# Performance work log

Measured on AMD Instinct MI355X. Metric: run time of the kernel, lower is better.

Reference implementation:

```python
import jax, jax.numpy as jnp
import numpy as np

B, D, T, H, CHUNK, MAX_REL = 4, 512, 8192, 8, 64, 2
HD = D // H


def setup_inputs() -> dict:
    key = jax.random.key(0)
    ks = jax.random.split(key, 16)
    s = 0.02
    inp = {
        "q": jax.random.normal(ks[0], (B, D, T), jnp.float32),
        "k": jax.random.normal(ks[1], (B, D, T), jnp.float32),
        "v": jax.random.normal(ks[2], (B, D, T), jnp.float32),
        "masks": jnp.ones((B, 1, T), jnp.float32),
        "Wq": jax.random.normal(ks[3], (D, D), jnp.float32) * s,
        "bq": jnp.zeros((D,), jnp.float32),
        "Wk": jax.random.normal(ks[4], (D, D), jnp.float32) * s,
        "bk": jnp.zeros((D,), jnp.float32),
        "Wv": jax.random.normal(ks[5], (D, D), jnp.float32) * s,
        "bv": jnp.zeros((D,), jnp.float32),
        "Wo": jax.random.normal(ks[6], (D, D), jnp.float32) * s,
        "bo": jnp.zeros((D,), jnp.float32),
        "rel_k": jax.random.normal(ks[7], (2 * MAX_REL + 1, HD), jnp.float32) * s,
        "rel_v": jax.random.normal(ks[8], (2 * MAX_REL + 1, HD), jnp.float32) * s,
    }
    return inp


def reference(q, k, v, masks, Wq, bq, Wk, bk, Wv, bv, Wo, bo, rel_k, rel_v):
    n = CHUNK
    g = T // n  # T is a multiple of chunck_size -> no padding branch
    bg = B * g

    # (B, D, T) -> (B, T, D) -> (B*g, n, D) chunking
    qt = jnp.swapaxes(q, 1, 2).reshape(bg, n, D)
    kt = jnp.swapaxes(k, 1, 2).reshape(bg, n, D)
    vt = jnp.swapaxes(v, 1, 2).reshape(bg, n, D)
    cm = jnp.swapaxes(masks, 1, 2).reshape(bg, n)  # per-chunk mask values

    # gen_key_padding_mask: chunks that are entirely zero are un-masked (set to 1)
    all_zero = jnp.sum(cm, axis=-1) == 0.0
    cm_fixed = jnp.where(all_zero[:, None], 1.0, cm)
    kpm = cm_fixed == 0.0  # (bg, n) True = masked key

    # projections (torch Linear: x @ W.T + b)
    qp = qt @ Wq.T + bq
    kp = kt @ Wk.T + bk
    vp = vt @ Wv.T + bv

    qh = qp.reshape(bg, n, H, HD).transpose(0, 2, 1, 3)  # (bg, H, n, hd)
    kh = kp.reshape(bg, n, H, HD).transpose(0, 2, 1, 3)
    vh = vp.reshape(bg, n, H, HD).transpose(0, 2, 1, 3)

    # content-content scores
    attn1 = jnp.einsum('bhqd,bhkd->bhqk', qh, kh)

    # relative position indices: clip(k - q, -max, max) + max
    ridx = jnp.clip(jnp.arange(n)[None, :] - jnp.arange(n)[:, None], -MAX_REL, MAX_REL) + MAX_REL
    rk = rel_k[ridx]  # (n, n, hd)
    rv = rel_v[ridx]  # (n, n, hd)

    # content-position scores
    attn2 = jnp.einsum('bhqd,qkd->bhqk', qh, rk)

    scale = jnp.sqrt(jnp.asarray(HD, jnp.float32))
    attn = (attn1 + attn2) / scale
    attn = jnp.where(kpm[:, None, None, :], -jnp.inf, attn)
    p = jax.nn.softmax(attn, axis=-1)  # (bg, H, n, n)

    w1 = jnp.einsum('bhqk,bhkd->bhqd', p, vh)
    w2 = jnp.einsum('bhqk,qkd->bhqd', p, rv)
    xo = (w1 + w2).transpose(0, 2, 1, 3).reshape(bg, n, D)
    xo = xo @ Wo.T + bo

    out = xo.reshape(B, T, D)
    out = jnp.swapaxes(out, 1, 2)  # (B, D, T)
    return out * masks
```

## Files before the change

### kernel.cpp

```cpp
#include <hip/hip_runtime.h>


typedef __attribute__((ext_vector_type(8))) short short8;
typedef __attribute__((ext_vector_type(4))) float f32x4;
typedef __attribute__((ext_vector_type(2))) unsigned int uint2v;
typedef __attribute__((ext_vector_type(4))) unsigned short ushort4v;

#define DEV static __device__ __forceinline__

DEV unsigned short f2bf(float f) {
  union { float f; unsigned int u; } x; x.f = f;
  unsigned int r = x.u + 0x7fffu + ((x.u >> 16) & 1u);
  return (unsigned short)(r >> 16);
}
DEV float bf2f(unsigned short h) {
  union { unsigned int u; float f; } x; x.u = ((unsigned int)h) << 16;
  return x.f;
}

constexpr int Bn = 4, Dm = 512, Tn = 8192, NC = 64;
constexpr int Gn = Tn / NC;
constexpr int BG = Bn * Gn;
constexpr int WSZ = Dm * Dm;
constexpr size_t XTSZ = (size_t)Bn * Tn * Dm;

__global__ __launch_bounds__(256) void wcvt_tiled(
    const float* __restrict__ wq, const float* __restrict__ wk,
    const float* __restrict__ wv, const float* __restrict__ wo,
    unsigned short* __restrict__ dst) {
  int i = blockIdx.x * 256 + threadIdx.x;
  int m = i >> 16, fi = i & 65535;
  int o = fi >> 7, d = (fi & 127) << 2;
  const float* src = (m == 0) ? wq : (m == 1) ? wk : (m == 2) ? wv : wo;
  f32x4 v = *(const f32x4*)(src + o * Dm + d);
  ushort4v u;
  u[0] = f2bf(v[0]); u[1] = f2bf(v[1]); u[2] = f2bf(v[2]); u[3] = f2bf(v[3]);
  int doff = m * WSZ + ((o >> 6) << 15) + ((d >> 5) << 11) + ((o & 63) << 5) + (d & 31);
  *(ushort4v*)(dst + doff) = u;
}

__global__ __launch_bounds__(256) void xpose_kernel(
    const float* __restrict__ q, const float* __restrict__ k,
    const float* __restrict__ v, unsigned short* __restrict__ xt) {
  __shared__ unsigned short tile[64 * 65];
  const int tid = threadIdx.x, bid = blockIdx.x;
  const int tz = bid >> 12, rem = bid & 4095;
  const int cid = rem >> 3, dh = rem & 7;
  const int b = cid >> 7, t0 = (cid & 127) * 64, d0 = dh * 64;
  const float* xin = (tz == 0) ? q : (tz == 1) ? k : v;
  const int lane = tid & 63, drow = tid >> 6;
  const size_t base = (size_t)b * Dm * Tn + t0 + lane;
#pragma unroll
  for (int p = 0; p < 16; ++p) {
    int dr = drow + p * 4;
    float f = xin[base + (size_t)(d0 + dr) * Tn];
    tile[lane * 65 + dr] = f2bf(f);
  }
  __syncthreads();
  unsigned short* xb = xt + (size_t)tz * XTSZ + ((size_t)cid << 15) + (dh << 12);
  const int t = tid >> 2, dlo = (tid & 3) * 8;
#pragma unroll
  for (int h = 0; h < 2; ++h) {
    short8 s;
#pragma unroll
    for (int j = 0; j < 8; ++j) s[j] = (short)tile[t * 65 + h * 32 + dlo + j];
    *(short8*)(xb + h * 2048 + t * 32 + dlo) = s;
  }
}

__global__ __launch_bounds__(512, 2)
void fused2_kernel(const unsigned short* __restrict__ xt,
                   const float* __restrict__ masks,
                   const unsigned short* __restrict__ wbf,
                   const float* __restrict__ bq, const float* __restrict__ bk,
                   const float* __restrict__ bv, const float* __restrict__ bo,
                   const float* __restrict__ relk, const float* __restrict__ relv,
                   float* __restrict__ out)
{
  extern __shared__ char lds[];
  const int tid  = threadIdx.x;
  const int lane = tid & 63;
  const int w    = tid >> 6;
  const int l15  = lane & 15;
  const int lg   = lane >> 4;
  const int c    = blockIdx.x;
  const int b    = c >> 7;
  const int t0   = (c & (Gn - 1)) * NC;

  char* regA = lds + w * 16384;
  char* regB = regA + 8192;

  float cmv = masks[(size_t)b * Tn + t0 + lane];
  unsigned long long nzb = __ballot(cmv != 0.0f);
  unsigned long long kpm = (nzb == 0ull) ? 0ull : __ballot(cmv == 0.0f);

  const f32x4 fzero = {0.f, 0.f, 0.f, 0.f};
  const int aoff = l15 * 32 + lg * 8;
  const unsigned short* xq = xt + ((size_t)c << 15);
  const unsigned short* xk = xq + XTSZ;
  const unsigned short* xv = xq + 2 * XTSZ;

  auto project = [&](const unsigned short* __restrict__ xb,
                     const unsigned short* __restrict__ wb, f32x4 (&acc)[4][4]) {
#pragma unroll
    for (int mi = 0; mi < 4; ++mi)
#pragma unroll
      for (int ni = 0; ni < 4; ++ni) acc[mi][ni] = fzero;
#pragma unroll
    for (int kk = 0; kk < 16; ++kk) {
      short8 af[4], bf_[4];
#pragma unroll
      for (int mi = 0; mi < 4; ++mi)
        af[mi] = *(const short8*)(xb + kk * 2048 + mi * 512 + aoff);
#pragma unroll
      for (int ni = 0; ni < 4; ++ni)
        bf_[ni] = *(const short8*)(wb + kk * 2048 + ni * 512 + aoff);
#pragma unroll
      for (int ni = 0; ni < 4; ++ni)
#pragma unroll
        for (int mi = 0; mi < 4; ++mi)
          acc[mi][ni] = __builtin_amdgcn_mfma_f32_16x16x32_bf16(af[mi], bf_[ni],
                                                                acc[mi][ni], 0, 0, 0);
    }
  };

  f32x4 acc[4][4];

  project(xq, wbf + 0 * WSZ + w * 32768, acc);
#pragma unroll
  for (int ni = 0; ni < 4; ++ni) {
    float bia = bq[64 * w + ni * 16 + l15];
    int hd = ni * 16 + l15;
#pragma unroll
    for (int mi = 0; mi < 4; ++mi)
#pragma unroll
      for (int rr = 0; rr < 4; ++rr) {
        int t = mi * 16 + lg * 4 + rr;
        int off = (t * 128 + hd * 2) ^ ((t & 7) << 4);
        *(unsigned short*)(regA + off) = f2bf(acc[mi][ni][rr] + bia);
      }
  }

  project(xk, wbf + 1 * WSZ + w * 32768, acc);
#pragma unroll
  for (int ni = 0; ni < 4; ++ni) {
    float bia = bk[64 * w + ni * 16 + l15];
    int hd = ni * 16 + l15;
#pragma unroll
    for (int mi = 0; mi < 4; ++mi)
// ... 119 lines not shown
#pragma unroll
    for (int ni = 0; ni < 4; ++ni) oacc[mi][ni] = fzero;
#pragma unroll
  for (int kk = 0; kk < 2; ++kk) {
    short8 av[4], bp[4];
#pragma unroll
    for (int mi = 0; mi < 4; ++mi) {
      int row = mi * 16 + l15;
      int off = (row * 128 + (kk * 32 + lg * 8) * 2) ^ ((row & 7) << 4);
      av[mi] = *(const short8*)(regA + off);
      bp[mi] = *(const short8*)(regB + off);
    }
#pragma unroll
    for (int ni = 0; ni < 4; ++ni)
#pragma unroll
      for (int mi = 0; mi < 4; ++mi)
        oacc[mi][ni] = __builtin_amdgcn_mfma_f32_16x16x32_bf16(av[mi], bp[ni],
                                                               oacc[mi][ni], 0, 0, 0);
  }

  float psh0[4], psh1[4], psh2[4], psh3[4], psh4[4];
#pragma unroll
  for (int ni = 0; ni < 4; ++ni) {
    int qt2 = ni * 16 + l15;
    psh0[ni] = __shfl(ps0, qt2); psh1[ni] = __shfl(ps1, qt2); psh2[ni] = __shfl(ps2, qt2);
    psh3[ni] = __shfl(ps3, qt2); psh4[ni] = __shfl(ps4, qt2);
  }
  uint2v xop[4][4];
#pragma unroll
  for (int mi = 0; mi < 4; ++mi) {
    float rv_[4][5];
#pragma unroll
    for (int rr = 0; rr < 4; ++rr) {
      int hd = mi * 16 + lg * 4 + rr;
#pragma unroll
      for (int r = 0; r < 5; ++r) rv_[rr][r] = relv[r * 64 + hd];
    }
#pragma unroll
    for (int ni = 0; ni < 4; ++ni) {
      unsigned short u[4];
#pragma unroll
      for (int rr = 0; rr < 4; ++rr) {
        float w2 = psh0[ni] * rv_[rr][0] + psh1[ni] * rv_[rr][1] + psh2[ni] * rv_[rr][2]
                 + psh3[ni] * rv_[rr][3] + psh4[ni] * rv_[rr][4];
        u[rr] = f2bf(oacc[mi][ni][rr] + w2);
      }
      uint2v pk; pk[0] = u[0] | ((unsigned int)u[1] << 16);
      pk[1] = u[2] | ((unsigned int)u[3] << 16);
      xop[mi][ni] = pk;
    }
  }

  __syncthreads();
  char* xobuf = lds;
#pragma unroll
  for (int ni = 0; ni < 4; ++ni) {
    int t = ni * 16 + l15;
#pragma unroll
    for (int mi = 0; mi < 4; ++mi) {
      int d = 64 * w + mi * 16 + lg * 4;
      int off = (t * 1024 + d * 2) ^ ((t & 15) << 4);
      *(uint2v*)(xobuf + off) = xop[mi][ni];
    }
  }
  __syncthreads();

  f32x4 cacc[4][4];
#pragma unroll
  for (int mi = 0; mi < 4; ++mi)
#pragma unroll
    for (int ni = 0; ni < 4; ++ni) cacc[mi][ni] = fzero;
  const unsigned short* wob = wbf + 3 * WSZ + w * 32768;
#pragma unroll
  for (int kk = 0; kk < 16; ++kk) {
    short8 ax[4], bw[4];
#pragma unroll
    for (int mi = 0; mi < 4; ++mi) {
      int t = mi * 16 + l15;
      int off = (t * 1024 + (kk * 32 + lg * 8) * 2) ^ ((t & 15) << 4);
      ax[mi] = *(const short8*)(xobuf + off);
    }
#pragma unroll
    for (int ni = 0; ni < 4; ++ni)
      bw[ni] = *(const short8*)(wob + kk * 2048 + ni * 512 + aoff);
#pragma unroll
    for (int ni = 0; ni < 4; ++ni)
#pragma unroll
      for (int mi = 0; mi < 4; ++mi)
        cacc[mi][ni] = __builtin_amdgcn_mfma_f32_16x16x32_bf16(ax[mi], bw[ni],
                                                               cacc[mi][ni], 0, 0, 0);
  }
#pragma unroll
  for (int mi = 0; mi < 4; ++mi) {
    int tl = mi * 16 + lg * 4;
    f32x4 mv = *(const f32x4*)(masks + (size_t)b * Tn + t0 + tl);
#pragma unroll
    for (int ni = 0; ni < 4; ++ni) {
      int o = 64 * w + ni * 16 + l15;
      float bia = bo[o];
      f32x4 r;
#pragma unroll
      for (int rr = 0; rr < 4; ++rr) r[rr] = (cacc[mi][ni][rr] + bia) * mv[rr];
      *(f32x4*)(out + ((size_t)b * Dm + o) * Tn + t0 + tl) = r;
    }
  }
}

__global__ void wcvt_kernel(const float* __restrict__ wq, const float* __restrict__ wk,
                            const float* __restrict__ wv, const float* __restrict__ wo,
                            unsigned short* __restrict__ dst) {
  int i = (blockIdx.x * blockDim.x + threadIdx.x) * 4;
  const float* src = (i < WSZ) ? wq : (i < 2 * WSZ) ? wk : (i < 3 * WSZ) ? wv : wo;
  int off = i & (WSZ - 1);
  f32x4 v = *(const f32x4*)(src + off);
  ushort4v o;
  o[0] = f2bf(v[0]); o[1] = f2bf(v[1]); o[2] = f2bf(v[2]); o[3] = f2bf(v[3]);
  *(ushort4v*)(dst + i) = o;
}

__global__ __launch_bounds__(512, 2)
void fused_kernel(const float* __restrict__ qx, const float* __restrict__ kx,
                  const float* __restrict__ vx, const float* __restrict__ masks,
                  const unsigned short* __restrict__ wbf,
                  const float* __restrict__ bq, const float* __restrict__ bk,
                  const float* __restrict__ bv, const float* __restrict__ bo,
                  const float* __restrict__ relk, const float* __restrict__ relv,
                  float* __restrict__ out)
{
  extern __shared__ char lds[];
  const int tid  = threadIdx.x;
  const int lane = tid & 63;
  const int w    = tid >> 6;
  const int l15  = lane & 15;
  const int lg   = lane >> 4;
  const int c    = blockIdx.x;
  const int b    = c >> 7;
  const int t0   = (c & (Gn - 1)) * NC;

  char* xbuf = lds;
  char* regA = lds + 16 * 1024 + w * 16 * 1024;
  char* regB = regA + 8 * 1024;

  float cmv = masks[(size_t)b * Tn + t0 + lane];
  unsigned long long nzb = __ballot(cmv != 0.0f);
  unsigned long long kpm = (nzb == 0ull) ? 0ull : __ballot(cmv == 0.0f);

  const f32x4 fzero = {0.f, 0.f, 0.f, 0.f};

  auto project = [&](const float* __restrict__ xin, const unsigned short* __restrict__ Wp,
                     f32x4 (&acc)[4][4]) {
#pragma unroll
    for (int mi = 0; mi < 4; ++mi)
#pragma unroll
      for (int ni = 0; ni < 4; ++ni) acc[mi][ni] = fzero;
    const size_t xbase = (size_t)b * Dm * Tn + t0 + lane;
    for (int s = 0; s < 4; ++s) {
      const int d0 = s * 128;
      short8 xs[2];
#pragma unroll
      for (int cc = 0; cc < 2; ++cc)
#pragma unroll
        for (int j = 0; j < 8; ++j) {
          float f = xin[xbase + (size_t)(d0 + 16 * w + 8 * cc + j) * Tn];
          xs[cc][j] = (short)f2bf(f);
        }
      short8 wf[4][4];
#pragma unroll
      for (int ni = 0; ni < 4; ++ni)
#pragma unroll
        for (int kk = 0; kk < 4; ++kk) {
          int o = 64 * w + ni * 16 + l15;
          int d = d0 + kk * 32 + lg * 8;
          wf[ni][kk] = *(const short8*)(Wp + o * Dm + d);
        }
      __syncthreads();
#pragma unroll
      for (int cc = 0; cc < 2; ++cc) {
        int off = (lane * 256 + (16 * w + 8 * cc) * 2) ^ ((lane & 15) << 4);
        *(short8*)(xbuf + off) = xs[cc];
      }
      __syncthreads();
#pragma unroll
      for (int kk = 0; kk < 4; ++kk) {
        short8 af[4];
#pragma unroll
        for (int mi = 0; mi < 4; ++mi) {
          int t = mi * 16 + l15;
          int off = (t * 256 + (kk * 32 + lg * 8) * 2) ^ ((t & 15) << 4);
          af[mi] = *(const short8*)(xbuf + off);
        }
#pragma unroll
        for (int ni = 0; ni < 4; ++ni)
#pragma unroll
          for (int mi = 0; mi < 4; ++mi)
            acc[mi][ni] = __builtin_amdgcn_mfma_f32_16x16x32_bf16(af[mi], wf[ni][kk],
                                                                  acc[mi][ni], 0, 0, 0);
      }
    }
  };

  f32x4 acc[4][4];

  project(qx, wbf + 0 * WSZ, acc);
#pragma unroll
  for (int ni = 0; ni < 4; ++ni) {
    float bia = bq[64 * w + ni * 16 + l15];
    int hd = ni * 16 + l15;
#pragma unroll
    for (int mi = 0; mi < 4; ++mi)
#pragma unroll
      for (int rr = 0; rr < 4; ++rr) {
        int t = mi * 16 + lg * 4 + rr;
        int off = (t * 128 + hd * 2) ^ ((t & 7) << 4);
        *(unsigned short*)(regA + off) = f2bf(acc[mi][ni][rr] + bia);
      }
  }

  project(kx, wbf + 1 * WSZ, acc);
#pragma unroll
  for (int ni = 0; ni < 4; ++ni) {
    float bia = bk[64 * w + ni * 16 + l15];
    int hd = ni * 16 + l15;
#pragma unroll
    for (int mi = 0; mi < 4; ++mi)
#pragma unroll
      for (int rr = 0; rr < 4; ++rr) {
        int t = mi * 16 + lg * 4 + rr;
        int off = (t * 128 + hd * 2) ^ ((t & 7) << 4);
        *(unsigned short*)(regB + off) = f2bf(acc[mi][ni][rr] + bia);
      }
  }

  f32x4 sacc[4][4];
#pragma unroll
  for (int mi = 0; mi < 4; ++mi)
#pragma unroll
    for (int ni = 0; ni < 4; ++ni) sacc[mi][ni] = fzero;
#pragma unroll
  for (int kk = 0; kk < 2; ++kk) {
    short8 aq[4], bkf[4];
#pragma unroll
    for (int mi = 0; mi < 4; ++mi) {
      int t = mi * 16 + l15;
      int off = (t * 128 + (kk * 32 + lg * 8) * 2) ^ ((t & 7) << 4);
      aq[mi]  = *(const short8*)(regA + off);
      bkf[mi] = *(const short8*)(regB + off);
    }
#pragma unroll
    for (int ni = 0; ni < 4; ++ni)
#pragma unroll
      for (int mi = 0; mi < 4; ++mi)
        sacc[mi][ni] = __builtin_amdgcn_mfma_f32_16x16x32_bf16(aq[mi], bkf[ni],
                                                               sacc[mi][ni], 0, 0, 0);
  }

  float qr0 = 0, qr1 = 0, qr2 = 0, qr3 = 0, qr4 = 0;
#pragma unroll
  for (int g = 0; g < 8; ++g) {
    short8 q8 = *(const short8*)(regA + ((lane * 128 + g * 16) ^ ((lane & 7) << 4)));
#pragma unroll
    for (int j = 0; j < 8; ++j) {
      float qf = bf2f((unsigned short)q8[j]);
      qr0 += qf * relk[0 * 64 + g * 8 + j];
      qr1 += qf * relk[1 * 64 + g * 8 + j];
      qr2 += qf * relk[2 * 64 + g * 8 + j];
      qr3 += qf * relk[3 * 64 + g * 8 + j];
      qr4 += qf * relk[4 * 64 + g * 8 + j];
    }
  }

  const float scale = 0.125f;
#pragma unroll
  for (int mi = 0; mi < 4; ++mi)
#pragma unroll
    for (int rr = 0; rr < 4; ++rr) {
      int qt = mi * 16 + lg * 4 + rr;
      float q0 = __shfl(qr0, qt), q1 = __shfl(qr1, qt), q2 = __shfl(qr2, qt),
            q3 = __shfl(qr3, qt), q4 = __shfl(qr4, qt);
      float sv[4];
#pragma unroll
      for (int ni = 0; ni < 4; ++ni) {
        int kt = ni * 16 + l15;
        int dd = kt - qt;
        float a2 = (dd <= -2) ? q0 : (dd == -1) ? q1 : (dd == 0) ? q2 : (dd == 1) ? q3 : q4;
        float s = (sacc[mi][ni][rr] + a2) * scale;
        if ((kpm >> kt) & 1ull) s = -1e30f;
        sv[ni] = s;
      }
      float m = fmaxf(fmaxf(sv[0], sv[1]), fmaxf(sv[2], sv[3]));
#pragma unroll
      for (int xm = 1; xm < 16; xm <<= 1) m = fmaxf(m, __shfl_xor(m, xm));
      float ssum = 0.f;
#pragma unroll
      for (int ni = 0; ni < 4; ++ni) { sv[ni] = __expf(sv[ni] - m); ssum += sv[ni]; }
#pragma unroll
      for (int xm = 1; xm < 16; xm <<= 1) ssum += __shfl_xor(ssum, xm);
      float inv = 1.0f / ssum;
#pragma unroll
      for (int ni = 0; ni < 4; ++ni) {
        int kt = ni * 16 + l15;
        int off = (qt * 128 + kt * 2) ^ ((qt & 7) << 4);
        *(unsigned short*)(regB + off) = f2bf(sv[ni] * inv);
      }
    }

  float ps0 = 0, ps1 = 0, ps2 = 0, ps3 = 0, tot = 0;
#pragma unroll
  for (int g = 0; g < 8; ++g) {
    short8 p8 = *(const short8*)(regB + ((lane * 128 + g * 16) ^ ((lane & 7) << 4)));
#pragma unroll
    for (int j = 0; j < 8; ++j) {
      int kt = g * 8 + j;
      float p = bf2f((unsigned short)p8[j]);
      int dd = kt - lane;
      tot += p;
      ps0 += (dd <= -2) ? p : 0.f;
      ps1  = (dd == -1) ? p : ps1;
      ps2  = (dd ==  0) ? p : ps2;
      ps3  = (dd ==  1) ? p : ps3;
    }
  }
  float ps4 = tot - ps0 - ps1 - ps2 - ps3;

  project(vx, wbf + 2 * WSZ, acc);
#pragma unroll
  for (int ni = 0; ni < 4; ++ni) {
    float bia = bv[64 * w + ni * 16 + l15];
    int hd = ni * 16 + l15;
#pragma unroll
    for (int mi = 0; mi < 4; ++mi) {
      unsigned int lo = (unsigned int)f2bf(acc[mi][ni][0] + bia) |
                        ((unsigned int)f2bf(acc[mi][ni][1] + bia) << 16);
      unsigned int hi = (unsigned int)f2bf(acc[mi][ni][2] + bia) |
                        ((unsigned int)f2bf(acc[mi][ni][3] + bia) << 16);
      uint2v pk; pk[0] = lo; pk[1] = hi;
      int off = (hd * 128 + (mi * 16 + lg * 4) * 2) ^ ((hd & 7) << 4);
      *(uint2v*)(regA + off) = pk;
    }
  }

  f32x4 oacc[4][4];
#pragma unroll
  for (int mi = 0; mi < 4; ++mi)
#pragma unroll
    for (int ni = 0; ni < 4; ++ni) oacc[mi][ni] = fzero;
#pragma unroll
  for (int kk = 0; kk < 2; ++kk) {
    short8 av[4], bp[4];
#pragma unroll
    for (int mi = 0; mi < 4; ++mi) {
      int row = mi * 16 + l15;
      int off = (row * 128 + (kk * 32 + lg * 8) * 2) ^ ((row & 7) << 4);
      av[mi] = *(const short8*)(regA + off);
      bp[mi] = *(const short8*)(regB + off);
    }
#pragma unroll
    for (int ni = 0; ni < 4; ++ni)
#pragma unroll
      for (int mi = 0; mi < 4; ++mi)
        oacc[mi][ni] = __builtin_amdgcn_mfma_f32_16x16x32_bf16(av[mi], bp[ni],
                                                               oacc[mi][ni], 0, 0, 0);
  }

  float psh0[4], psh1[4], psh2[4], psh3[4], psh4[4];
#pragma unroll
  for (int ni = 0; ni < 4; ++ni) {
    int qt2 = ni * 16 + l15;
    psh0[ni] = __shfl(ps0, qt2); psh1[ni] = __shfl(ps1, qt2); psh2[ni] = __shfl(ps2, qt2);
    psh3[ni] = __shfl(ps3, qt2); psh4[ni] = __shfl(ps4, qt2);
  }
  uint2v xop[4][4];
#pragma unroll
  for (int mi = 0; mi < 4; ++mi) {
    float rv_[4][5];
#pragma unroll
    for (int rr = 0; rr < 4; ++rr) {
      int hd = mi * 16 + lg * 4 + rr;
#pragma unroll
      for (int r = 0; r < 5; ++r) rv_[rr][r] = relv[r * 64 + hd];
    }
#pragma unroll
    for (int ni = 0; ni < 4; ++ni) {
      unsigned short u[4];
#pragma unroll
      for (int rr = 0; rr < 4; ++rr) {
        float w2 = psh0[ni] * rv_[rr][0] + psh1[ni] * rv_[rr][1] + psh2[ni] * rv_[rr][2]
                 + psh3[ni] * rv_[rr][3] + psh4[ni] * rv_[rr][4];
        u[rr] = f2bf(oacc[mi][ni][rr] + w2);
      }
      uint2v pk; pk[0] = u[0] | ((unsigned int)u[1] << 16);
      pk[1] = u[2] | ((unsigned int)u[3] << 16);
      xop[mi][ni] = pk;
    }
  }

  __syncthreads();
  char* xobuf = lds + 16 * 1024;
#pragma unroll
  for (int ni = 0; ni < 4; ++ni) {
    int t = ni * 16 + l15;
#pragma unroll
    for (int mi = 0; mi < 4; ++mi) {
      int d = 64 * w + mi * 16 + lg * 4;
      int off = (t * 1024 + d * 2) ^ ((t & 15) << 4);
      *(uint2v*)(xobuf + off) = xop[mi][ni];
    }
  }
  __syncthreads();

  f32x4 cacc[4][4];
#pragma unroll
  for (int mi = 0; mi < 4; ++mi)
#pragma unroll
    for (int ni = 0; ni < 4; ++ni) cacc[mi][ni] = fzero;
  const unsigned short* Wo = wbf + 3 * WSZ;
#pragma unroll
  for (int kk = 0; kk < 16; ++kk) {
    short8 ax[4], bw[4];
#pragma unroll
    for (int mi = 0; mi < 4; ++mi) {
      int t = mi * 16 + l15;
      int off = (t * 1024 + (kk * 32 + lg * 8) * 2) ^ ((t & 15) << 4);
      ax[mi] = *(const short8*)(xobuf + off);
    }
#pragma unroll
    for (int ni = 0; ni < 4; ++ni) {
      int o = 64 * w + ni * 16 + l15;
      bw[ni] = *(const short8*)(Wo + o * Dm + kk * 32 + lg * 8);
    }
#pragma unroll
    for (int ni = 0; ni < 4; ++ni)
#pragma unroll
      for (int mi = 0; mi < 4; ++mi)
        cacc[mi][ni] = __builtin_amdgcn_mfma_f32_16x16x32_bf16(ax[mi], bw[ni],
                                                               cacc[mi][ni], 0, 0, 0);
  }
#pragma unroll
  for (int mi = 0; mi < 4; ++mi) {
    int tl = mi * 16 + lg * 4;
    f32x4 mv = *(const f32x4*)(masks + (size_t)b * Tn + t0 + tl);
#pragma unroll
    for (int ni = 0; ni < 4; ++ni) {
      int o = 64 * w + ni * 16 + l15;
      float bia = bo[o];
      f32x4 r;
#pragma unroll
      for (int rr = 0; rr < 4; ++rr) r[rr] = (cacc[mi][ni][rr] + bia) * mv[rr];
      *(f32x4*)(out + ((size_t)b * Dm + o) * Tn + t0 + tl) = r;
    }
  }
}

extern "C" void kernel_launch(void* const* d_in, const int* in_sizes, int n_in,
                              void* d_out, int out_size, void* d_ws, size_t ws_size,
                              hipStream_t stream) {
  (void)in_sizes; (void)n_in; (void)out_size;
  const float* q  = (const float*)d_in[0];
  const float* k  = (const float*)d_in[1];
  const float* v  = (const float*)d_in[2];
  const float* ms = (const float*)d_in[3];
  const float* Wq = (const float*)d_in[4];
  const float* bq = (const float*)d_in[5];
  const float* Wk = (const float*)d_in[6];
  const float* bk = (const float*)d_in[7];
  const float* Wv = (const float*)d_in[8];
  const float* bv = (const float*)d_in[9];
  const float* Wo = (const float*)d_in[10];
  const float* bo = (const float*)d_in[11];
  const float* rk = (const float*)d_in[12];
  const float* rv = (const float*)d_in[13];
  float* out = (float*)d_out;

  unsigned short* wbf = (unsigned short*)d_ws;
  const size_t need = (size_t)4 * WSZ * 2 + 3 * XTSZ * 2;

  if (ws_size >= need) {
    unsigned short* xt = wbf + 4 * WSZ;
    wcvt_tiled<<<dim3(1024), dim3(256), 0, stream>>>(Wq, Wk, Wv, Wo, wbf);
    xpose_kernel<<<dim3(12288), dim3(256), 0, stream>>>(q, k, v, xt);
    hipFuncSetAttribute((const void*)fused2_kernel,
                        hipFuncAttributeMaxDynamicSharedMemorySize, 131072);
    fused2_kernel<<<dim3(BG), dim3(512), 131072, stream>>>(xt, ms, wbf,
                                                           bq, bk, bv, bo, rk, rv, out);
  } else {
    wcvt_kernel<<<dim3(1024), dim3(256), 0, stream>>>(Wq, Wk, Wv, Wo, wbf);
    hipFuncSetAttribute((const void*)fused_kernel,
                        hipFuncAttributeMaxDynamicSharedMemorySize, 147456);
    fused_kernel<<<dim3(BG), dim3(512), 147456, stream>>>(q, k, v, ms, wbf,
                                                          bq, bk, bv, bo, rk, rv, out);
  }
}
```

Before: 210.6 us.

## Split fused attention into per-head attention kernel and separate output GEMM

Result: slower. 257.4 us (+22.2%).

```diff
diff --git a/kernel.cpp b/kernel.cpp
--- a/kernel.cpp
+++ b/kernel.cpp
@@ -16,6 +16,12 @@
 DEV float bf2f(unsigned short h) {
   union { unsigned int u; float f; } x; x.u = ((unsigned int)h) << 16;
   return x.f;
+}
+
+DEV void gload16(char* lds, const void* g) {
+  __builtin_amdgcn_global_load_lds(
+      (const __attribute__((address_space(1))) unsigned int*)g,
+      (__attribute__((address_space(3))) unsigned int*)lds, 16, 0, 0);
 }
 
 constexpr int Bn = 4, Dm = 512, Tn = 8192, NC = 64;
@@ -23,6 +29,20 @@
 constexpr int BG = Bn * Gn;
 constexpr int WSZ = Dm * Dm;
 constexpr size_t XTSZ = (size_t)Bn * Tn * Dm;
+constexpr size_t XOSZ = (size_t)Bn * Tn * Dm;
+
+__global__ __launch_bounds__(256) void wcvt_kernel(
+    const float* __restrict__ wq, const float* __restrict__ wk,
+    const float* __restrict__ wv, const float* __restrict__ wo,
+    unsigned short* __restrict__ dst) {
+  int i = (blockIdx.x * blockDim.x + threadIdx.x) * 4;
+  const float* src = (i < WSZ) ? wq : (i < 2 * WSZ) ? wk : (i < 3 * WSZ) ? wv : wo;
+  int off = i & (WSZ - 1);
+  f32x4 v = *(const f32x4*)(src + off);
+  ushort4v o;
+  o[0] = f2bf(v[0]); o[1] = f2bf(v[1]); o[2] = f2bf(v[2]); o[3] = f2bf(v[3]);
+  *(ushort4v*)(dst + i) = o;
+}
 
 __global__ __launch_bounds__(256) void wcvt_tiled(
     const float* __restrict__ wq, const float* __restrict__ wk,
@@ -65,6 +85,341 @@
 #pragma unroll
     for (int j = 0; j < 8; ++j) s[j] = (short)tile[t * 65 + h * 32 + dlo + j];
     *(short8*)(xb + h * 2048 + t * 32 + dlo) = s;
+  }
+}
+
+__global__ __launch_bounds__(64, 2)
+void attn_kernel(const unsigned short* __restrict__ xt,
+                 const float* __restrict__ masks,
+                 const unsigned short* __restrict__ wbf,
+                 const float* __restrict__ bq, const float* __restrict__ bk,
+                 const float* __restrict__ bv,
+                 const float* __restrict__ relk, const float* __restrict__ relv,
+                 unsigned short* __restrict__ xo)
+{
+  __shared__ char ldsbuf[16384];
+  char* regA = ldsbuf;
+  char* regB = ldsbuf + 8192;
+  const int lane = threadIdx.x;
+  const int l15 = lane & 15, lg = lane >> 4;
+  const int bid = blockIdx.x;
+  const int c = bid & 511;
+  const int h = bid >> 9;
+  const int b = c >> 7, t0 = (c & 127) * 64;
+
+  float cmv = masks[(size_t)b * Tn + t0 + lane];
+  unsigned long long nzb = __ballot(cmv != 0.0f);
+  unsigned long long kpm = (nzb == 0ull) ? 0ull : __ballot(cmv == 0.0f);
+
+  const f32x4 fzero = {0.f, 0.f, 0.f, 0.f};
+  const int aoff = l15 * 32 + lg * 8;
+  const unsigned short* xq = xt + ((size_t)c << 15);
+  const unsigned short* xk = xq + XTSZ;
+  const unsigned short* xv = xq + 2 * XTSZ;
+  const unsigned short* wq = wbf + 0 * WSZ + (h * 64) * Dm;
+  const unsigned short* wk = wbf + 1 * WSZ + (h * 64) * Dm;
+  const unsigned short* wv = wbf + 2 * WSZ + (h * 64) * Dm;
+  const int woff = l15 * Dm + lg * 8;
+
+  f32x4 qa[4][4], ka[4][4];
+#pragma unroll
+  for (int mi = 0; mi < 4; ++mi)
+#pragma unroll
+    for (int ni = 0; ni < 4; ++ni) { qa[mi][ni] = fzero; ka[mi][ni] = fzero; }
+#pragma unroll
+  for (int kk = 0; kk < 16; ++kk) {
+    short8 axq[4], axk[4], bwq[4], bwk[4];
+#pragma unroll
+    for (int mi = 0; mi < 4; ++mi) {
+      axq[mi] = *(const short8*)(xq + kk * 2048 + mi * 512 + aoff);
+      axk[mi] = *(const short8*)(xk + kk * 2048 + mi * 512 + aoff);
+    }
+#pragma unroll
+    for (int ni = 0; ni < 4; ++ni) {
+      bwq[ni] = *(const short8*)(wq + ni * 16 * Dm + woff + kk * 32);
+      bwk[ni] = *(const short8*)(wk + ni * 16 * Dm + woff + kk * 32);
+    }
+#pragma unroll
+    for (int ni = 0; ni < 4; ++ni)
+#pragma unroll
+      for (int mi = 0; mi < 4; ++mi) {
+        qa[mi][ni] = __builtin_amdgcn_mfma_f32_16x16x32_bf16(axq[mi], bwq[ni], qa[mi][ni], 0, 0, 0);
+        ka[mi][ni] = __builtin_amdgcn_mfma_f32_16x16x32_bf16(axk[mi], bwk[ni], ka[mi][ni], 0, 0, 0);
+      }
+  }
+#pragma unroll
+  for (int ni = 0; ni < 4; ++ni) {
+    float biq = bq[64 * h + ni * 16 + l15];
+    float bik = bk[64 * h + ni * 16 + l15];
+    int hd = ni * 16 + l15;
+#pragma unroll
+    for (int mi = 0; mi < 4; ++mi)
+#pragma unroll
+      for (int rr = 0; rr < 4; ++rr) {
+        int t = mi * 16 + lg * 4 + rr;
+        int off = (t * 128 + hd * 2) ^ ((t & 7) << 4);
+        *(unsigned short*)(regA + off) = f2bf(qa[mi][ni][rr] + biq);
+        *(unsigned short*)(regB + off) = f2bf(ka[mi][ni][rr] + bik);
+      }
+  }
+
+  f32x4 sacc[4][4];
+#pragma unroll
+  for (int mi = 0; mi < 4; ++mi)
+#pragma unroll
+    for (int ni = 0; ni < 4; ++ni) sacc[mi][ni] = fzero;
+#pragma unroll
+  for (int kk = 0; kk < 2; ++kk) {
+    short8 aq[4], bkf[4];
+#pragma unroll
+    for (int mi = 0; mi < 4; ++mi) {
+      int t = mi * 16 + l15;
+      int off = (t * 128 + (kk * 32 + lg * 8) * 2) ^ ((t & 7) << 4);
+      aq[mi]  = *(const short8*)(regA + off);
+      bkf[mi] = *(const short8*)(regB + off);
+    }
+#pragma unroll
+    for (int ni = 0; ni < 4; ++ni)
+#pragma unroll
+      for (int mi = 0; mi < 4; ++mi)
+        sacc[mi][ni] = __builtin_amdgcn_mfma_f32_16x16x32_bf16(aq[mi], bkf[ni], sacc[mi][ni], 0, 0, 0);
+  }
+
+  float qr0 = 0, qr1 = 0, qr2 = 0, qr3 = 0, qr4 = 0;
+#pragma unroll
+  for (int g = 0; g < 8; ++g) {
+    short8 q8 = *(const short8*)(regA + ((lane * 128 + g * 16) ^ ((lane & 7) << 4)));
+#pragma unroll
+    for (int j = 0; j < 8; ++j) {
+      float qf = bf2f((unsigned short)q8[j]);
+      qr0 += qf * relk[0 * 64 + g * 8 + j];
+      qr1 += qf * relk[1 * 64 + g * 8 + j];
+      qr2 += qf * relk[2 * 64 + g * 8 + j];
+      qr3 += qf * relk[3 * 64 + g * 8 + j];
+      qr4 += qf * relk[4 * 64 + g * 8 + j];
+    }
+  }
+
+  f32x4 vacc[4][4];
+#pragma unroll
+  for (int mi = 0; mi < 4; ++mi)
+#pragma unroll
+    for (int ni = 0; ni < 4; ++ni) vacc[mi][ni] = fzero;
+#pragma unroll
+  for (int kk = 0; kk < 16; ++kk) {
+    short8 af[4], bf_[4];
+#pragma unroll
+    for (int mi = 0; mi < 4; ++mi)
+      af[mi] = *(const short8*)(xv + kk * 2048 + mi * 512 + aoff);
+#pragma unroll
+    for (int ni = 0; ni < 4; ++ni)
+      bf_[ni] = *(const short8*)(wv + ni * 16 * Dm + woff + kk * 32);
+#pragma unroll
+    for (int ni = 0; ni < 4; ++ni)
+#pragma unroll
+      for (int mi = 0; mi < 4; ++mi)
+        vacc[mi][ni] = __builtin_amdgcn_mfma_f32_16x16x32_bf16(af[mi], bf_[ni], vacc[mi][ni], 0, 0, 0);
+  }
+#pragma unroll
+  for (int ni = 0; ni < 4; ++ni) {
+    float bia = bv[64 * h + ni * 16 + l15];
+    int hd = ni * 16 + l15;
+#pragma unroll
+    for (int mi = 0; mi < 4; ++mi) {
+      unsigned int lo = (unsigned int)f2bf(vacc[mi][ni][0] + bia) |
+                        ((unsigned int)f2bf(vacc[mi][ni][1] + bia) << 16);
+      unsigned int hi = (unsigned int)f2bf(vacc[mi][ni][2] + bia) |
+                        ((unsigned int)f2bf(vacc[mi][ni][3] + bia) << 16);
+      uint2v pk; pk[0] = lo; pk[1] = hi;
+      int off = (hd * 128 + (mi * 16 + lg * 4) * 2) ^ ((hd & 7) << 4);
+      *(uint2v*)(regA + off) = pk;
+    }
+  }
+
+  const float scale = 0.125f;
+#pragma unroll
+  for (int mi = 0; mi < 4; ++mi)
+#pragma unroll
+    for (int rr = 0; rr < 4; ++rr) {
+      int qt = mi * 16 + lg * 4 + rr;
+      float q0 = __shfl(qr0, qt), q1 = __shfl(qr1, qt), q2 = __shfl(qr2, qt),
+            q3 = __shfl(qr3, qt), q4 = __shfl(qr4, qt);
+      float sv[4];
+#pragma unroll
+      for (int ni = 0; ni < 4; ++ni) {
+        int kt = ni * 16 + l15;
+        int dd = kt - qt;
+        float a2 = (dd <= -2) ? q0 : (dd == -1) ? q1 : (dd == 0) ? q2 : (dd == 1) ? q3 : q4;
+        float s = (sacc[mi][ni][rr] + a2) * scale;
+        if ((kpm >> kt) & 1ull) s = -1e30f;
+        sv[ni] = s;
+      }
+      float m = fmaxf(fmaxf(sv[0], sv[1]), fmaxf(sv[2], sv[3]));
+#pragma unroll
+      for (int xm = 1; xm < 16; xm <<= 1) m = fmaxf(m, __shfl_xor(m, xm));
+      float ssum = 0.f;
+#pragma unroll
+      for (int ni = 0; ni < 4; ++ni) { sv[ni] = __expf(sv[ni] - m); ssum += sv[ni]; }
+#pragma unroll
+      for (int xm = 1; xm < 16; xm <<= 1) ssum += __shfl_xor(ssum, xm);
+      float inv = 1.0f / ssum;
+#pragma unroll
+      for (int ni = 0; ni < 4; ++ni) {
+        int kt = ni * 16 + l15;
+        int off = (qt * 128 + kt * 2) ^ ((qt & 7) << 4);
+        *(unsigned short*)(regB + off) = f2bf(sv[ni] * inv);
+      }
+    }
+
+  float ps0 = 0, ps1 = 0, ps2 = 0, ps3 = 0, tot = 0;
+#pragma unroll
+  for (int g = 0; g < 8; ++g) {
+    short8 p8 = *(const short8*)(regB + ((lane * 128 + g * 16) ^ ((lane & 7) << 4)));
+#pragma unroll
+    for (int j = 0; j < 8; ++j) {
+      int kt = g * 8 + j;
+      float p = bf2f((unsigned short)p8[j]);
+      int dd = kt - lane;
+      tot += p;
+      ps0 += (dd <= -2) ? p : 0.f;
+      ps1  = (dd == -1) ? p : ps1;
+      ps2  = (dd ==  0) ? p : ps2;
+      ps3  = (dd ==  1) ? p : ps3;
+    }
+  }
+  float ps4 = tot - ps0 - ps1 - ps2 - ps3;
+
+  f32x4 oacc[4][4];
+#pragma unroll
+  for (int mi = 0; mi < 4; ++mi)
+#pragma unroll
+    for (int ni = 0; ni < 4; ++ni) oacc[mi][ni] = fzero;
+#pragma unroll
+  for (int kk = 0; kk < 2; ++kk) {
+    short8 av[4], bp[4];
+#pragma unroll
+    for (int mi = 0; mi < 4; ++mi) {
+      int row = mi * 16 + l15;
+      int off = (row * 128 + (kk * 32 + lg * 8) * 2) ^ ((row & 7) << 4);
+      av[mi] = *(const short8*)(regA + off);
+      bp[mi] = *(const short8*)(regB + off);
+    }
+#pragma unroll
+    for (int ni = 0; ni < 4; ++ni)
+#pragma unroll
+      for (int mi = 0; mi < 4; ++mi)
+        oacc[mi][ni] = __builtin_amdgcn_mfma_f32_16x16x32_bf16(av[mi], bp[ni], oacc[mi][ni], 0, 0, 0);
+  }
+
+  float psh0[4], psh1[4], psh2[4], psh3[4], psh4[4];
+#pragma unroll
+  for (int ni = 0; ni < 4; ++ni) {
+    int qt2 = ni * 16 + l15;
+    psh0[ni] = __shfl(ps0, qt2); psh1[ni] = __shfl(ps1, qt2); psh2[ni] = __shfl(ps2, qt2);
+    psh3[ni] = __shfl(ps3, qt2); psh4[ni] = __shfl(ps4, qt2);
+  }
+#pragma unroll
+  for (int mi = 0; mi < 4; ++mi) {
+    float rv_[4][5];
+#pragma unroll
+    for (int rr = 0; rr < 4; ++rr) {
+      int hd = mi * 16 + lg * 4 + rr;
+#pragma unroll
+      for (int r = 0; r < 5; ++r) rv_[rr][r] = relv[r * 64 + hd];
+    }
+#pragma unroll
+    for (int ni = 0; ni < 4; ++ni) {
+      unsigned short u[4];
+#pragma unroll
+      for (int rr = 0; rr < 4; ++rr) {
+        float w2 = psh0[ni] * rv_[rr][0] + psh1[ni] * rv_[rr][1] + psh2[ni] * rv_[rr][2]
+                 + psh3[ni] * rv_[rr][3] + psh4[ni] * rv_[rr][4];
+        u[rr] = f2bf(oacc[mi][ni][rr] + w2);
+      }
+      uint2v pk; pk[0] = u[0] | ((unsigned int)u[1] << 16);
+      pk[1] = u[2] | ((unsigned int)u[3] << 16);
+      int t = ni * 16 + l15;
+      int off = (t * 128 + (mi * 16 + lg * 4) * 2) ^ ((t & 7) << 4);
+      *(uint2v*)(regB + off) = pk;
+    }
+  }
+
+#pragma unroll
+  for (int it = 0; it < 8; ++it) {
+    int p = it * 64 + lane;
+    int row = p >> 3, c16 = p & 7;
+    short8 val = *(const short8*)(regB + ((row * 128 + c16 * 16) ^ ((row & 7) << 4)));
+    *(short8*)(xo + (size_t)(c * 64 + row) * Dm + h * 64 + c16 * 8) = val;
+  }
+}
+
+__global__ __launch_bounds__(256, 2)
+void outgemm_kernel(const unsigned short* __restrict__ xo,
+                    const unsigned short* __restrict__ wo,
+                    const float* __restrict__ masks, const float* __restrict__ bo,
+                    float* __restrict__ out)
+{
+  __shared__ char lA[16384], lB[16384];
+  const int tid = threadIdx.x;
+  const int lane = tid & 63, w = tid >> 6;
+  const int wm = w >> 1, wn = w & 1;
+  const int l15 = lane & 15, lg = lane >> 4;
+  const int bidx = blockIdx.x;
+  const int n0 = (bidx & 3) * 128, m0 = (bidx >> 2) * 128;
+
+  f32x4 acc[4][4];
+  const f32x4 fzero = {0.f, 0.f, 0.f, 0.f};
+#pragma unroll
+  for (int mi = 0; mi < 4; ++mi)
+#pragma unroll
+    for (int ni = 0; ni < 4; ++ni) acc[mi][ni] = fzero;
+
+  for (int k0 = 0; k0 < 512; k0 += 64) {
+#pragma unroll
+    for (int it = 0; it < 4; ++it) {
+      int slot = it * 256 + w * 64 + lane;
+      int row = slot >> 3, c16 = slot & 7;
+      int gcol = k0 + ((c16 ^ (row & 7)) * 8);
+      gload16(lA + it * 4096 + w * 1024, xo + (size_t)(m0 + row) * Dm + gcol);
+      gload16(lB + it * 4096 + w * 1024, wo + (size_t)(n0 + row) * Dm + gcol);
+    }
+    __syncthreads();
+#pragma unroll
+    for (int kk = 0; kk < 2; ++kk) {
+      short8 af[4], bf_[4];
+#pragma unroll
+      for (int mi = 0; mi < 4; ++mi) {
+        int m = wm * 64 + mi * 16 + l15;
+        af[mi] = *(const short8*)(lA + ((m * 128 + (kk * 32 + lg * 8) * 2) ^ ((m & 7) << 4)));
+      }
+#pragma unroll
+      for (int ni = 0; ni < 4; ++ni) {
+        int n = wn * 64 + ni * 16 + l15;
+        bf_[ni] = *(const short8*)(lB + ((n * 128 + (kk * 32 + lg * 8) * 2) ^ ((n & 7) << 4)));
+      }
+#pragma unroll
+      for (int ni = 0; ni < 4; ++ni)
+#pragma unroll
+        for (int mi = 0; mi < 4; ++mi)
+          acc[mi][ni] = __builtin_amdgcn_mfma_f32_16x16x32_bf16(af[mi], bf_[ni], acc[mi][ni], 0, 0, 0);
+    }
+    __syncthreads();
+  }
+
+#pragma unroll
+  for (int mi = 0; mi < 4; ++mi) {
+    int tg = m0 + wm * 64 + mi * 16 + lg * 4;
+    int b = tg >> 13, t = tg & (Tn - 1);
+    f32x4 mv = *(const f32x4*)(masks + (size_t)b * Tn + t);
+#pragma unroll
+    for (int ni = 0; ni < 4; ++ni) {
+      int o = n0 + wn * 64 + ni * 16 + l15;
+      float bia = bo[o];
+      f32x4 r;
+#pragma unroll
+      for (int rr = 0; rr < 4; ++rr) r[rr] = (acc[mi][ni][rr] + bia) * mv[rr];
+      *(f32x4*)(out + ((size_t)b * Dm + o) * Tn + t) = r;
+    }
   }
 }
 
@@ -350,352 +705,7 @@
     }
 #pragma unroll
     for (int ni = 0; ni < 4; ++ni)
-      bw[ni] = *(const short8*)(wob + kk * 2048 + ni * 512 + aoff);
-#pragma unroll
-    for (int ni = 0; ni < 4; ++ni)
-#pragma unroll
-      for (int mi = 0; mi < 4; ++mi)
-        cacc[mi][ni] = __builtin_amdgcn_mfma_f32_16x16x32_bf16(ax[mi], bw[ni],
-                                                               cacc[mi][ni], 0, 0, 0);
-  }
-#pragma unroll
-  for (int mi = 0; mi < 4; ++mi) {
-    int tl = mi * 16 + lg * 4;
-    f32x4 mv = *(const f32x4*)(masks + (size_t)b * Tn + t0 + tl);
-#pragma unroll
-    for (int ni = 0; ni < 4; ++ni) {
-      int o = 64 * w + ni * 16 + l15;
-      float bia = bo[o];
-      f32x4 r;
-#pragma unroll
-      for (int rr = 0; rr < 4; ++rr) r[rr] = (cacc[mi][ni][rr] + bia) * mv[rr];
-      *(f32x4*)(out + ((size_t)b * Dm + o) * Tn + t0 + tl) = r;
-    }
-  }
-}
-
-__global__ void wcvt_kernel(const float* __restrict__ wq, const float* __restrict__ wk,
-                            const float* __restrict__ wv, const float* __restrict__ wo,
-                            unsigned short* __restrict__ dst) {
-  int i = (blockIdx.x * blockDim.x + threadIdx.x) * 4;
-  const float* src = (i < WSZ) ? wq : (i < 2 * WSZ) ? wk : (i < 3 * WSZ) ? wv : wo;
-  int off = i & (WSZ - 1);
-  f32x4 v = *(const f32x4*)(src + off);
-  ushort4v o;
-  o[0] = f2bf(v[0]); o[1] = f2bf(v[1]); o[2] = f2bf(v[2]); o[3] = f2bf(v[3]);
-  *(ushort4v*)(dst + i) = o;
-}
-
-__global__ __launch_bounds__(512, 2)
-void fused_kernel(const float* __restrict__ qx, const float* __restrict__ kx,
-                  const float* __restrict__ vx, const float* __restrict__ masks,
-                  const unsigned short* __restrict__ wbf,
-                  const float* __restrict__ bq, const float* __restrict__ bk,
-                  const float* __restrict__ bv, const float* __restrict__ bo,
-                  const float* __restrict__ relk, const float* __restrict__ relv,
-                  float* __restrict__ out)
-{
-  extern __shared__ char lds[];
-  const int tid  = threadIdx.x;
-  const int lane = tid & 63;
-  const int w    = tid >> 6;
-  const int l15  = lane & 15;
-  const int lg   = lane >> 4;
-  const int c    = blockIdx.x;
-  const int b    = c >> 7;
-  const int t0   = (c & (Gn - 1)) * NC;
-
-  char* xbuf = lds;
-  char* regA = lds + 16 * 1024 + w * 16 * 1024;
-  char* regB = regA + 8 * 1024;
-
-  float cmv = masks[(size_t)b * Tn + t0 + lane];
-  unsigned long long nzb = __ballot(cmv != 0.0f);
-  unsigned long long kpm = (nzb == 0ull) ? 0ull : __ballot(cmv == 0.0f);
-
-  const f32x4 fzero = {0.f, 0.f, 0.f, 0.f};
-
-  auto project = [&](const float* __restrict__ xin, const unsigned short* __restrict__ Wp,
-                     f32x4 (&acc)[4][4]) {
-#pragma unroll
-    for (int mi = 0; mi < 4; ++mi)
-#pragma unroll
-      for (int ni = 0; ni < 4; ++ni) acc[mi][ni] = fzero;
-    const size_t xbase = (size_t)b * Dm * Tn + t0 + lane;
-    for (int s = 0; s < 4; ++s) {
-      const int d0 = s * 128;
-      short8 xs[2];
-#pragma unroll
-      for (int cc = 0; cc < 2; ++cc)
-#pragma unroll
-        for (int j = 0; j < 8; ++j) {
-          float f = xin[xbase + (size_t)(d0 + 16 * w + 8 * cc + j) * Tn];
-          xs[cc][j] = (short)f2bf(f);
-        }
-      short8 wf[4][4];
-#pragma unroll
-      for (int ni = 0; ni < 4; ++ni)
-#pragma unroll
-        for (int kk = 0; kk < 4; ++kk) {
-          int o = 64 * w + ni * 16 + l15;
-          int d = d0 + kk * 32 + lg * 8;
-          wf[ni][kk] = *(const short8*)(Wp + o * Dm + d);
-        }
-      __syncthreads();
-#pragma unroll
-      for (int cc = 0; cc < 2; ++cc) {
-        int off = (lane * 256 + (16 * w + 8 * cc) * 2) ^ ((lane & 15) << 4);
-        *(short8*)(xbuf + off) = xs[cc];
-      }
-      __syncthreads();
-#pragma unroll
-      for (int kk = 0; kk < 4; ++kk) {
-        short8 af[4];
-#pragma unroll
-        for (int mi = 0; mi < 4; ++mi) {
-          int t = mi * 16 + l15;
-          int off = (t * 256 + (kk * 32 + lg * 8) * 2) ^ ((t & 15) << 4);
-          af[mi] = *(const short8*)(xbuf + off);
-        }
-#pragma unroll
-        for (int ni = 0; ni < 4; ++ni)
-#pragma unroll
-          for (int mi = 0; mi < 4; ++mi)
-            acc[mi][ni] = __builtin_amdgcn_mfma_f32_16x16x32_bf16(af[mi], wf[ni][kk],
-                                                                  acc[mi][ni], 0, 0, 0);
-      }
-    }
-  };
-
-  f32x4 acc[4][4];
-
-  project(qx, wbf + 0 * WSZ, acc);
-#pragma unroll
-  for (int ni = 0; ni < 4; ++ni) {
-    float bia = bq[64 * w + ni * 16 + l15];
-    int hd = ni * 16 + l15;
-#pragma unroll
-    for (int mi = 0; mi < 4; ++mi)
-#pragma unroll
-      for (int rr = 0; rr < 4; ++rr) {
-        int t = mi * 16 + lg * 4 + rr;
-        int off = (t * 128 + hd * 2) ^ ((t & 7) << 4);
-        *(unsigned short*)(regA + off) = f2bf(acc[mi][ni][rr] + bia);
-      }
-  }
-
-  project(kx, wbf + 1 * WSZ, acc);
-#pragma unroll
-  for (int ni = 0; ni < 4; ++ni) {
-    float bia = bk[64 * w + ni * 16 + l15];
-    int hd = ni * 16 + l15;
-#pragma unroll
-    for (int mi = 0; mi < 4; ++mi)
-#pragma unroll
-      for (int rr = 0; rr < 4; ++rr) {
-        int t = mi * 16 + lg * 4 + rr;
-        int off = (t * 128 + hd * 2) ^ ((t & 7) << 4);
-        *(unsigned short*)(regB + off) = f2bf(acc[mi][ni][rr] + bia);
-      }
-  }
-
-  f32x4 sacc[4][4];
-#pragma unroll
-  for (int mi = 0; mi < 4; ++mi)
-#pragma unroll
-    for (int ni = 0; ni < 4; ++ni) sacc[mi][ni] = fzero;
-#pragma unroll
-  for (int kk = 0; kk < 2; ++kk) {
-    short8 aq[4], bkf[4];
-#pragma unroll
-    for (int mi = 0; mi < 4; ++mi) {
-      int t = mi * 16 + l15;
-      int off = (t * 128 + (kk * 32 + lg * 8) * 2) ^ ((t & 7) << 4);
-      aq[mi]  = *(const short8*)(regA + off);
-      bkf[mi] = *(const short8*)(regB + off);
-    }
-#pragma unroll
-    for (int ni = 0; ni < 4; ++ni)
-#pragma unroll
-      for (int mi = 0; mi < 4; ++mi)
-        sacc[mi][ni] = __builtin_amdgcn_mfma_f32_16x16x32_bf16(aq[mi], bkf[ni],
-                                                               sacc[mi][ni], 0, 0, 0);
-  }
-
-  float qr0 = 0, qr1 = 0, qr2 = 0, qr3 = 0, qr4 = 0;
-#pragma unroll
-  for (int g = 0; g < 8; ++g) {
-    short8 q8 = *(const short8*)(regA + ((lane * 128 + g * 16) ^ ((lane & 7) << 4)));
-#pragma unroll
-    for (int j = 0; j < 8; ++j) {
-      float qf = bf2f((unsigned short)q8[j]);
-      qr0 += qf * relk[0 * 64 + g * 8 + j];
-      qr1 += qf * relk[1 * 64 + g * 8 + j];
-      qr2 += qf * relk[2 * 64 + g * 8 + j];
-      qr3 += qf * relk[3 * 64 + g * 8 + j];
-      qr4 += qf * relk[4 * 64 + g * 8 + j];
-    }
-  }
-
-  const float scale = 0.125f;
-#pragma unroll
-  for (int mi = 0; mi < 4; ++mi)
-#pragma unroll
-    for (int rr = 0; rr < 4; ++rr) {
-      int qt = mi * 16 + lg * 4 + rr;
-      float q0 = __shfl(qr0, qt), q1 = __shfl(qr1, qt), q2 = __shfl(qr2, qt),
-            q3 = __shfl(qr3, qt), q4 = __shfl(qr4, qt);
-      float sv[4];
-#pragma unroll
-      for (int ni = 0; ni < 4; ++ni) {
-        int kt = ni * 16 + l15;
-        int dd = kt - qt;
-        float a2 = (dd <= -2) ? q0 : (dd == -1) ? q1 : (dd == 0) ? q2 : (dd == 1) ? q3 : q4;
-        float s = (sacc[mi][ni][rr] + a2) * scale;
-        if ((kpm >> kt) & 1ull) s = -1e30f;
-        sv[ni] = s;
-      }
-      float m = fmaxf(fmaxf(sv[0], sv[1]), fmaxf(sv[2], sv[3]));
-#pragma unroll
-      for (int xm = 1; xm < 16; xm <<= 1) m = fmaxf(m, __shfl_xor(m, xm));
-      float ssum = 0.f;
-#pragma unroll
-      for (int ni = 0; ni < 4; ++ni) { sv[ni] = __expf(sv[ni] - m); ssum += sv[ni]; }
-#pragma unroll
-      for (int xm = 1; xm < 16; xm <<= 1) ssum += __shfl_xor(ssum, xm);
-      float inv = 1.0f / ssum;
-#pragma unroll
-      for (int ni = 0; ni < 4; ++ni) {
-        int kt = ni * 16 + l15;
-        int off = (qt * 128 + kt * 2) ^ ((qt & 7) << 4);
-        *(unsigned short*)(regB + off) = f2bf(sv[ni] * inv);
-      }
-    }
-
-  float ps0 = 0, ps1 = 0, ps2 = 0, ps3 = 0, tot = 0;
-#pragma unroll
-  for (int g = 0; g < 8; ++g) {
-    short8 p8 = *(const short8*)(regB + ((lane * 128 + g * 16) ^ ((lane & 7) << 4)));
-#pragma unroll
-    for (int j = 0; j < 8; ++j) {
-      int kt = g * 8 + j;
-      float p = bf2f((unsigned short)p8[j]);
-      int dd = kt - lane;
-      tot += p;
-      ps0 += (dd <= -2) ? p : 0.f;
-      ps1  = (dd == -1) ? p : ps1;
-      ps2  = (dd ==  0) ? p : ps2;
-      ps3  = (dd ==  1) ? p : ps3;
-    }
-  }
-  float ps4 = tot - ps0 - ps1 - ps2 - ps3;
-
-  project(vx, wbf + 2 * WSZ, acc);
-#pragma unroll
-  for (int ni = 0; ni < 4; ++ni) {
-    float bia = bv[64 * w + ni * 16 + l15];
-    int hd = ni * 16 + l15;
-#pragma unroll
-    for (int mi = 0; mi < 4; ++mi) {
-      unsigned int lo = (unsigned int)f2bf(acc[mi][ni][0] + bia) |
-                        ((unsigned int)f2bf(acc[mi][ni][1] + bia) << 16);
-      unsigned int hi = (unsigned int)f2bf(acc[mi][ni][2] + bia) |
-                        ((unsigned int)f2bf(acc[mi][ni][3] + bia) << 16);
-      uint2v pk; pk[0] = lo; pk[1] = hi;
-      int off = (hd * 128 + (mi * 16 + lg * 4) * 2) ^ ((hd & 7) << 4);
-      *(uint2v*)(regA + off) = pk;
-    }
-  }
-
-  f32x4 oacc[4][4];
-#pragma unroll
-  for (int mi = 0; mi < 4; ++mi)
-#pragma unroll
-    for (int ni = 0; ni < 4; ++ni) oacc[mi][ni] = fzero;
-#pragma unroll
-  for (int kk = 0; kk < 2; ++kk) {
-    short8 av[4], bp[4];
-#pragma unroll
-    for (int mi = 0; mi < 4; ++mi) {
-      int row = mi * 16 + l15;
-      int off = (row * 128 + (kk * 32 + lg * 8) * 2) ^ ((row & 7) << 4);
-      av[mi] = *(const short8*)(regA + off);
-      bp[mi] = *(const short8*)(regB + off);
-    }
-#pragma unroll
-    for (int ni = 0; ni < 4; ++ni)
-#pragma unroll
-      for (int mi = 0; mi < 4; ++mi)
-        oacc[mi][ni] = __builtin_amdgcn_mfma_f32_16x16x32_bf16(av[mi], bp[ni],
-                                                               oacc[mi][ni], 0, 0, 0);
-  }
-
-  float psh0[4], psh1[4], psh2[4], psh3[4], psh4[4];
-#pragma unroll
-  for (int ni = 0; ni < 4; ++ni) {
-    int qt2 = ni * 16 + l15;
-    psh0[ni] = __shfl(ps0, qt2); psh1[ni] = __shfl(ps1, qt2); psh2[ni] = __shfl(ps2, qt2);
-    psh3[ni] = __shfl(ps3, qt2); psh4[ni] = __shfl(ps4, qt2);
-  }
-  uint2v xop[4][4];
-#pragma unroll
-  for (int mi = 0; mi < 4; ++mi) {
-    float rv_[4][5];
-#pragma unroll
-    for (int rr = 0; rr < 4; ++rr) {
-      int hd = mi * 16 + lg * 4 + rr;
-#pragma unroll
-      for (int r = 0; r < 5; ++r) rv_[rr][r] = relv[r * 64 + hd];
-    }
-#pragma unroll
-    for (int ni = 0; ni < 4; ++ni) {
-      unsigned short u[4];
-#pragma unroll
-      for (int rr = 0; rr < 4; ++rr) {
-        float w2 = psh0[ni] * rv_[rr][0] + psh1[ni] * rv_[rr][1] + psh2[ni] * rv_[rr][2]
-                 + psh3[ni] * rv_[rr][3] + psh4[ni] * rv_[rr][4];
-        u[rr] = f2bf(oacc[mi][ni][rr] + w2);
-      }
-      uint2v pk; pk[0] = u[0] | ((unsigned int)u[1] << 16);
-      pk[1] = u[2] | ((unsigned int)u[3] << 16);
-      xop[mi][ni] = pk;
-    }
-  }
-
-  __syncthreads();
-  char* xobuf = lds + 16 * 1024;
-#pragma unroll
-  for (int ni = 0; ni < 4; ++ni) {
-    int t = ni * 16 + l15;
-#pragma unroll
-    for (int mi = 0; mi < 4; ++mi) {
-      int d = 64 * w + mi * 16 + lg * 4;
-      int off = (t * 1024 + d * 2) ^ ((t & 15) << 4);
-      *(uint2v*)(xobuf + off) = xop[mi][ni];
-    }
-  }
-  __syncthreads();
-
-  f32x4 cacc[4][4];
-#pragma unroll
-  for (int mi = 0; mi < 4; ++mi)
-#pragma unroll
-    for (int ni = 0; ni < 4; ++ni) cacc[mi][ni] = fzero;
-  const unsigned short* Wo = wbf + 3 * WSZ;
-#pragma unroll
-  for (int kk = 0; kk < 16; ++kk) {
-    short8 ax[4], bw[4];
-#pragma unroll
-    for (int mi = 0; mi < 4; ++mi) {
-      int t = mi * 16 + l15;
-      int off = (t * 1024 + (kk * 32 + lg * 8) * 2) ^ ((t & 15) << 4);
-      ax[mi] = *(const short8*)(xobuf + off);
-    }
-#pragma unroll
-    for (int ni = 0; ni < 4; ++ni) {
-      int o = 64 * w + ni * 16 + l15;
-      bw[ni] = *(const short8*)(Wo + o * Dm + kk * 32 + lg * 8);
-    }
+      bw[ni] = *(const short8*)(wob + kk * 2048 + ni * 512 + l15 * 32 + lg * 8);
 #pragma unroll
     for (int ni = 0; ni < 4; ++ni)
 #pragma unroll
@@ -740,9 +750,19 @@
   float* out = (float*)d_out;
 
   unsigned short* wbf = (unsigned short*)d_ws;
-  const size_t need = (size_t)4 * WSZ * 2 + 3 * XTSZ * 2;
-
-  if (ws_size >= need) {
+  const size_t needA = ((size_t)4 * WSZ + 3 * XTSZ + XOSZ) * 2;
+  const size_t needB = ((size_t)4 * WSZ + 3 * XTSZ) * 2;
+
+  if (ws_size >= needA) {
+    unsigned short* xt = wbf + 4 * WSZ;
+    unsigned short* xo = xt + 3 * XTSZ;
+    wcvt_kernel<<<dim3(1024), dim3(256), 0, stream>>>(Wq, Wk, Wv, Wo, wbf);
+    xpose_kernel<<<dim3(12288), dim3(256), 0, stream>>>(q, k, v, xt);
+    attn_kernel<<<dim3(4096), dim3(64), 0, stream>>>(xt, ms, wbf, bq, bk, bv,
+                                                     rk, rv, xo);
+    outgemm_kernel<<<dim3(1024), dim3(256), 0, stream>>>(xo, wbf + 3 * WSZ,
+                                                         ms, bo, out);
+  } else {
     unsigned short* xt = wbf + 4 * WSZ;
     wcvt_tiled<<<dim3(1024), dim3(256), 0, stream>>>(Wq, Wk, Wv, Wo, wbf);
     xpose_kernel<<<dim3(12288), dim3(256), 0, stream>>>(q, k, v, xt);
@@ -750,11 +770,5 @@
                         hipFuncAttributeMaxDynamicSharedMemorySize, 131072);
     fused2_kernel<<<dim3(BG), dim3(512), 131072, stream>>>(xt, ms, wbf,
                                                            bq, bk, bv, bo, rk, rv, out);
-  } else {
-    wcvt_kernel<<<dim3(1024), dim3(256), 0, stream>>>(Wq, Wk, Wv, Wo, wbf);
-    hipFuncSetAttribute((const void*)fused_kernel,
-                        hipFuncAttributeMaxDynamicSharedMemorySize, 147456);
-    fused_kernel<<<dim3(BG), dim3(512), 147456, stream>>>(q, k, v, ms, wbf,
-                                                          bq, bk, bv, bo, rk, rv, out);
-  }
-}
+  }
+}
```
